# Kernel optimization log

Hardware: AMD Instinct MI355X
Metric: run time of the kernel (lower is better)

The kernel has to match this reference:

```python
import jax, jax.numpy as jnp
import numpy as np

ITERS = 3
EPS = 1e-6


def setup_inputs() -> dict:
    key = jax.random.key(0)
    k1, k2 = jax.random.split(key, 2)
    a = jax.random.normal(k1, (64, 1152, 1, 1, 1, 1), dtype=jnp.float32)
    v = jax.random.normal(k2, (64, 1152, 32, 4, 4, 1), dtype=jnp.float32)
    logits = jnp.ones((1, 1152, 32, 1, 1, 1), dtype=jnp.float32)
    return {"a": a, "v": v, "logits": logits}


def _squash(s):
    # s: (batch, 1, B, P, P, 1); norm over dim 2 (matches torch code, dim=2)
    norm_sq = jnp.sum(s * s, axis=2, keepdims=True)
    return jnp.sqrt(norm_sq + EPS) / (1.0 + norm_sq) * s


def reference(a, v, logits):
    # a: (batch, A, 1, 1, 1, 1) -- unused (overwritten in original forward)
    # v: (batch, A, B, P, P, 1); logits: (1, A, B, 1, 1, 1)
    batch = v.shape[0]
    b = jnp.broadcast_to(logits, (batch,) + logits.shape[1:])
    p = None
    for i in range(ITERS):
        c = jax.nn.softmax(b, axis=2)                    # route over B
        s = jnp.sum(c * v, axis=1, keepdims=True)        # (batch,1,B,P,P,1)
        p = _squash(s)
        if i < ITERS - 1:
            # agreement: sum over pose dims -> (batch, A, B, 1, 1, 1)
            b = b + jnp.sum(p * v, axis=(-3, -2, -1), keepdims=True)
    p = jnp.squeeze(p, axis=1)                           # (batch, B, P, P, 1)
    a_out = jnp.linalg.norm(p, ord=2, axis=2)            # (batch, B, P, 1)
    return (a_out, p)
```

## Files before the change

kernel.cpp:

```cpp
#include <hip/hip_runtime.h>
#include <math.h>

#define BATCH 64
#define ADIM  1152
#define BDIM  32
#define POSE  16
#define SLICE 512
#define CHUNKS 16
#define ROWS  72
#define RPW   18
#define WAVES 4
#define EPSQ  1e-6f
#define SPART_ITER ((size_t)BATCH * CHUNKS * SLICE)

typedef float v4f __attribute__((ext_vector_type(4)));

__device__ __forceinline__ unsigned pack_bf16x2(float a, float b) {
    unsigned ua = __float_as_uint(a), ub = __float_as_uint(b);
    ua = (ua + 0x7fffu + ((ua >> 16) & 1u)) >> 16;
    ub = (ub + 0x7fffu + ((ub >> 16) & 1u));
    return (ua & 0xffffu) | (ub & 0xffff0000u);
}

__device__ __forceinline__ v4f unpack_bf16x4(uint2 w) {
    v4f r;
    r.x = __uint_as_float(w.x << 16);
    r.y = __uint_as_float(w.x & 0xffff0000u);
    r.z = __uint_as_float(w.y << 16);
    r.w = __uint_as_float(w.y & 0xffff0000u);
    return r;
}

__global__ __launch_bounds__(256) void route0_compress(
    const float* __restrict__ v,
    const float* __restrict__ logits,
    uint2* __restrict__ tile,
    float* __restrict__ s_part)
{
    const int bt    = blockIdx.x >> 4;
    const int chunk = blockIdx.x & 15;
    const int t     = threadIdx.x;
    const int bc0   = (t >> 2) & 31;
    const int hi    = t >> 7;
    const int a0    = chunk * ROWS;

    __shared__ float w_sh[ROWS * BDIM];
    __shared__ v4f   red[128];

    if (t < ROWS) {
        const float* lr = logits + (size_t)(a0 + t) * BDIM;
        float s = 0.f;
        float e[BDIM];
#pragma unroll
        for (int b = 0; b < BDIM; ++b) { e[b] = __expf(lr[b]); s += e[b]; }
        float rd = 1.f / s;
#pragma unroll
        for (int b = 0; b < BDIM; ++b) w_sh[t * BDIM + b] = e[b] * rd;
    }
    __syncthreads();

    const v4f* vg = (const v4f*)(v + ((size_t)bt * ADIM + a0) * SLICE);
    uint2*     tg = tile + ((size_t)bt * ADIM + a0) * 128;

    v4f acc = (v4f){0.f, 0.f, 0.f, 0.f};
    v4f fA[6], fB[6];
#pragma unroll
    for (int u = 0; u < 6; ++u)
        fA[u] = __builtin_nontemporal_load(&vg[t + 256 * u]);

#pragma unroll
    for (int kk = 0; kk < 6; ++kk) {
        v4f* cur = (kk & 1) ? fB : fA;
        v4f* nxt = (kk & 1) ? fA : fB;
        if (kk + 1 < 6) {
#pragma unroll
            for (int u = 0; u < 6; ++u)
                nxt[u] = __builtin_nontemporal_load(&vg[t + 256 * ((kk + 1) * 6 + u)]);
        }
#pragma unroll
        for (int u = 0; u < 6; ++u) {
            const int k   = kk * 6 + u;
            const int i   = t + 256 * k;
            const int row = 2 * k + hi;
            tg[i] = make_uint2(pack_bf16x2(cur[u].x, cur[u].y),
                               pack_bf16x2(cur[u].z, cur[u].w));
            float c0 = w_sh[row * BDIM + bc0];
            acc += c0 * cur[u];
        }
    }

    __syncthreads();
    if (t >= 128) red[t - 128] = acc;
    __syncthreads();
    if (t < 128) {
        acc += red[t];
        ((v4f*)(s_part + ((size_t)bt * CHUNKS + chunk) * SLICE))[t] = acc;
    }
}

__global__ __launch_bounds__(256) void route_next(
    const uint2* __restrict__ tile,
    const float* __restrict__ logits,
    const float* __restrict__ psum_g,
    float* __restrict__ s_out)
{
    const int bt    = blockIdx.x >> 4;
    const int chunk = blockIdx.x & 15;
    const int t     = threadIdx.x;
    const int lane  = t & 63;
    const int wv    = t >> 6;
    const int bq    = lane >> 2;
    const int a0    = chunk * ROWS;

    __shared__ v4f red[WAVES * 128];

    const v4f* pp = (const v4f*)(psum_g + (size_t)bt * SLICE);
    v4f psA = pp[lane];
    v4f psB = pp[64 + lane];
    v4f acc0 = (v4f){0.f, 0.f, 0.f, 0.f};
    v4f acc1 = (v4f){0.f, 0.f, 0.f, 0.f};

    const int r0 = wv * RPW;
    const uint2* tb = tile + ((size_t)bt * ADIM + a0) * 128;

#pragma unroll 6
    for (int r = 0; r < RPW; ++r) {
        const int rw = r0 + r;
        uint2 wa = tb[rw * 128 + lane];
        uint2 wb = tb[rw * 128 + 64 + lane];
        v4f va = unpack_bf16x4(wa);
        v4f vb = unpack_bf16x4(wb);
        float b0 = logits[(size_t)(a0 + rw) * BDIM + bq];
        float b1 = logits[(size_t)(a0 + rw) * BDIM + 16 + bq];
        float d0 = psA.x * va.x + psA.y * va.y + psA.z * va.z + psA.w * va.w;
        float d1 = psB.x * vb.x + psB.y * vb.y + psB.z * vb.z + psB.w * vb.w;
        d0 += __shfl_xor(d0, 1, 64); d0 += __shfl_xor(d0, 2, 64);
        d1 += __shfl_xor(d1, 1, 64); d1 += __shfl_xor(d1, 2, 64);
        float e0 = __expf(b0 + d0);
        float e1 = __expf(b1 + d1);
        float uu = e0 + e1;
#pragma unroll
        for (int off = 4; off <= 32; off <<= 1)
            uu += __shfl_xor(uu, off, 64);
        float rd = __builtin_amdgcn_rcpf(uu);
        float c0 = e0 * rd, c1 = e1 * rd;
        acc0 += c0 * va;
        acc1 += c1 * vb;
    }

    __syncthreads();
    if (wv == 3) { red[lane] = acc0; red[64 + lane] = acc1; }
    __syncthreads();
    if (wv == 2) { red[lane] += acc0; red[64 + lane] += acc1; }
    __syncthreads();
    if (wv == 1) { red[lane] += acc0; red[64 + lane] += acc1; }
    __syncthreads();
    if (wv == 0) {
        v4f* sp = (v4f*)(s_out + ((size_t)bt * CHUNKS + chunk) * SLICE);
        sp[lane]      = red[lane] + acc0;
        sp[64 + lane] = red[64 + lane] + acc1;
    }
}

__global__ __launch_bounds__(512) void squash_pass(
    const float* __restrict__ s_part_j,
    float* __restrict__ psum,
    int add)
{
    const int bt = blockIdx.x;
    const int t  = threadIdx.x;

    __shared__ float sq[SLICE];
    __shared__ float fac[POSE];

    float sv = 0.f;
#pragma unroll
    for (int c = 0; c < CHUNKS; ++c)
        sv += s_part_j[((size_t)bt * CHUNKS + c) * SLICE + t];

    sq[t] = sv * sv;
    __syncthreads();
    if (t < POSE) {
        float n = 0.f;
        for (int b2 = 0; b2 < BDIM; ++b2) n += sq[b2 * POSE + t];
        fac[t] = sqrtf(n + EPSQ) / (1.f + n);
    }
    __syncthreads();
    float prev = add ? psum[(size_t)bt * SLICE + t] : 0.f;
    psum[(size_t)bt * SLICE + t] = prev + fac[t & 15] * sv;
}

__global__ __launch_bounds__(512) void final_out(
    const float* __restrict__ s_part2,
    float* __restrict__ out)
{
    const int bt = blockIdx.x;
    const int t  = threadIdx.x;
    const int pose = t & 15;

    __shared__ float sq[SLICE];
    __shared__ float ns[POSE];

    float sv = 0.f;
#pragma unroll
    for (int c = 0; c < CHUNKS; ++c)
        sv += s_part2[((size_t)bt * CHUNKS + c) * SLICE + t];

    sq[t] = sv * sv;
    __syncthreads();
    if (t < POSE) {
        float a = 0.f;
        for (int b2 = 0; b2 < BDIM; ++b2) a += sq[b2 * POSE + t];
        ns[t] = a;
    }
    __syncthreads();
    float n = ns[pose];
    float pv = sqrtf(n + EPSQ) / (1.f + n) * sv;

    out[8192 + (size_t)bt * SLICE + t] = pv;
    sq[t] = pv * pv;
    __syncthreads();
    if (t < 128) {
        const int b2 = t >> 2, p2 = t & 3;
        float a = 0.f;
#pragma unroll
        for (int p1 = 0; p1 < 4; ++p1) a += sq[b2 * POSE + p1 * 4 + p2];
        out[(size_t)bt * 128 + t] = sqrtf(a);
    }
}

extern "C" void kernel_launch(void* const* d_in, const int* in_sizes, int n_in,
                              void* d_out, int out_size, void* d_ws, size_t ws_size,
                              hipStream_t stream) {
    const float* v      = (const float*)d_in[1];
    const float* logits = (const float*)d_in[2];
    float* out = (float*)d_out;

    uint2* tile   = (uint2*)d_ws;
    float* s_part = (float*)((char*)d_ws + (size_t)BATCH * ADIM * 128 * sizeof(uint2));
    float* psum   = s_part + 3 * SPART_ITER;

    route0_compress<<<dim3(BATCH * CHUNKS), dim3(256), 0, stream>>>(
        v, logits, tile, s_part + 0 * SPART_ITER);
    squash_pass<<<dim3(BATCH), dim3(512), 0, stream>>>(
        s_part + 0 * SPART_ITER, psum, 0);
    route_next<<<dim3(BATCH * CHUNKS), dim3(256), 0, stream>>>(
        tile, logits, psum, s_part + 1 * SPART_ITER);
    squash_pass<<<dim3(BATCH), dim3(512), 0, stream>>>(
        s_part + 1 * SPART_ITER, psum, 1);
    route_next<<<dim3(BATCH * CHUNKS), dim3(256), 0, stream>>>(
        tile, logits, psum, s_part + 2 * SPART_ITER);
    final_out<<<dim3(BATCH), dim3(512), 0, stream>>>(
        s_part + 2 * SPART_ITER, out);
}
```

Measured before the change: 257.8 us.

## Drop bf16 tile cache and fuse squash into iteration passes reading fp32 v

Removes the bf16-compressed copy of v and has each routing iteration re-read the original fp32 v directly. The per-batch squash kernels are eliminated; each iteration block recomputes the squashed pose sums from the stored partial sums of prior iterations. This saves the compressed-tile write and two launches but doubles the bytes read per later iteration and adds redundant squash work per block. It also removes bf16 rounding of v.

```diff
diff --git a/kernel.cpp b/kernel.cpp
--- a/kernel.cpp
+++ b/kernel.cpp
@@ -4,105 +4,60 @@
 #define BATCH 64
 #define ADIM  1152
 #define BDIM  32
-#define POSE  16
 #define SLICE 512
 #define CHUNKS 16
 #define ROWS  72
 #define RPW   18
-#define WAVES 4
 #define EPSQ  1e-6f
 #define SPART_ITER ((size_t)BATCH * CHUNKS * SLICE)
 
 typedef float v4f __attribute__((ext_vector_type(4)));
 
-__device__ __forceinline__ unsigned pack_bf16x2(float a, float b) {
-    unsigned ua = __float_as_uint(a), ub = __float_as_uint(b);
-    ua = (ua + 0x7fffu + ((ua >> 16) & 1u)) >> 16;
-    ub = (ub + 0x7fffu + ((ub >> 16) & 1u));
-    return (ua & 0xffffu) | (ub & 0xffff0000u);
-}
-
-__device__ __forceinline__ v4f unpack_bf16x4(uint2 w) {
-    v4f r;
-    r.x = __uint_as_float(w.x << 16);
-    r.y = __uint_as_float(w.x & 0xffff0000u);
-    r.z = __uint_as_float(w.y << 16);
-    r.w = __uint_as_float(w.y & 0xffff0000u);
-    return r;
-}
-
-__global__ __launch_bounds__(256) void route0_compress(
+
+__device__ __forceinline__ void squash_from(const float* sp, int lane,
+                                            v4f& sA, v4f& sB, v4f& fac) {
+    const v4f* spv = (const v4f*)sp;
+    sA = (v4f){0.f, 0.f, 0.f, 0.f};
+    sB = (v4f){0.f, 0.f, 0.f, 0.f};
+#pragma unroll
+    for (int c = 0; c < CHUNKS; ++c) {
+        sA += spv[c * 128 + lane];
+        sB += spv[c * 128 + 64 + lane];
+    }
+    v4f nq = sA * sA + sB * sB;
+#pragma unroll
+    for (int off = 4; off <= 32; off <<= 1) {
+        nq.x += __shfl_xor(nq.x, off, 64);
+        nq.y += __shfl_xor(nq.y, off, 64);
+        nq.z += __shfl_xor(nq.z, off, 64);
+        nq.w += __shfl_xor(nq.w, off, 64);
+    }
+    fac.x = sqrtf(nq.x + EPSQ) / (1.f + nq.x);
+    fac.y = sqrtf(nq.y + EPSQ) / (1.f + nq.y);
+    fac.z = sqrtf(nq.z + EPSQ) / (1.f + nq.z);
+    fac.w = sqrtf(nq.w + EPSQ) / (1.f + nq.w);
+}
+
+__device__ __forceinline__ void reduce_write(v4f* red, int lane, int wv,
+                                             v4f ra, v4f rb, float* dst) {
+    __syncthreads();
+    if (wv == 3) { red[lane] = ra; red[64 + lane] = rb; }
+    __syncthreads();
+    if (wv == 2) { red[lane] += ra; red[64 + lane] += rb; }
+    __syncthreads();
+    if (wv == 1) { red[lane] += ra; red[64 + lane] += rb; }
+    __syncthreads();
+    if (wv == 0) {
+        v4f* sp = (v4f*)dst;
+        sp[lane]      = red[lane] + ra;
+        sp[64 + lane] = red[64 + lane] + rb;
+    }
+}
+
+__global__ __launch_bounds__(256) void pass0(
     const float* __restrict__ v,
     const float* __restrict__ logits,
-    uint2* __restrict__ tile,
-    float* __restrict__ s_part)
-{
-    const int bt    = blockIdx.x >> 4;
-    const int chunk = blockIdx.x & 15;
-    const int t     = threadIdx.x;
-    const int bc0   = (t >> 2) & 31;
-    const int hi    = t >> 7;
-    const int a0    = chunk * ROWS;
-
-    __shared__ float w_sh[ROWS * BDIM];
-    __shared__ v4f   red[128];
-
-    if (t < ROWS) {
-        const float* lr = logits + (size_t)(a0 + t) * BDIM;
-        float s = 0.f;
-        float e[BDIM];
-#pragma unroll
-        for (int b = 0; b < BDIM; ++b) { e[b] = __expf(lr[b]); s += e[b]; }
-        float rd = 1.f / s;
-#pragma unroll
-        for (int b = 0; b < BDIM; ++b) w_sh[t * BDIM + b] = e[b] * rd;
-    }
-    __syncthreads();
-
-    const v4f* vg = (const v4f*)(v + ((size_t)bt * ADIM + a0) * SLICE);
-    uint2*     tg = tile + ((size_t)bt * ADIM + a0) * 128;
-
-    v4f acc = (v4f){0.f, 0.f, 0.f, 0.f};
-    v4f fA[6], fB[6];
-#pragma unroll
-    for (int u = 0; u < 6; ++u)
-        fA[u] = __builtin_nontemporal_load(&vg[t + 256 * u]);
-
-#pragma unroll
-    for (int kk = 0; kk < 6; ++kk) {
-        v4f* cur = (kk & 1) ? fB : fA;
-        v4f* nxt = (kk & 1) ? fA : fB;
-        if (kk + 1 < 6) {
-#pragma unroll
-            for (int u = 0; u < 6; ++u)
-                nxt[u] = __builtin_nontemporal_load(&vg[t + 256 * ((kk + 1) * 6 + u)]);
-        }
-#pragma unroll
-        for (int u = 0; u < 6; ++u) {
-            const int k   = kk * 6 + u;
-            const int i   = t + 256 * k;
-            const int row = 2 * k + hi;
-            tg[i] = make_uint2(pack_bf16x2(cur[u].x, cur[u].y),
-                               pack_bf16x2(cur[u].z, cur[u].w));
-            float c0 = w_sh[row * BDIM + bc0];
-            acc += c0 * cur[u];
-        }
-    }
-
-    __syncthreads();
-    if (t >= 128) red[t - 128] = acc;
-    __syncthreads();
-    if (t < 128) {
-        acc += red[t];
-        ((v4f*)(s_part + ((size_t)bt * CHUNKS + chunk) * SLICE))[t] = acc;
-    }
-}
-
-__global__ __launch_bounds__(256) void route_next(
-    const uint2* __restrict__ tile,
-    const float* __restrict__ logits,
-    const float* __restrict__ psum_g,
-    float* __restrict__ s_out)
+    float* __restrict__ s0)
 {
     const int bt    = blockIdx.x >> 4;
     const int chunk = blockIdx.x & 15;
@@ -111,29 +66,101 @@
     const int wv    = t >> 6;
     const int bq    = lane >> 2;
     const int a0    = chunk * ROWS;
-
-    __shared__ v4f red[WAVES * 128];
-
-    const v4f* pp = (const v4f*)(psum_g + (size_t)bt * SLICE);
-    v4f psA = pp[lane];
-    v4f psB = pp[64 + lane];
+    const int r0    = wv * RPW;
+
+    __shared__ float w_sh[ROWS * BDIM];
+    __shared__ v4f   red[128];
+
+    if (t < ROWS) {
+        const float* lr = logits + (size_t)(a0 + t) * BDIM;
+        float e[BDIM];
+        float s = 0.f;
+#pragma unroll
+        for (int b = 0; b < BDIM; ++b) { e[b] = __expf(lr[b]); s += e[b]; }
+        float rd = 1.f / s;
+#pragma unroll
+        for (int b = 0; b < BDIM; ++b) w_sh[t * BDIM + b] = e[b] * rd;
+    }
+    __syncthreads();
+
+    const v4f* vg = (const v4f*)(v + ((size_t)bt * ADIM + a0 + r0) * SLICE);
     v4f acc0 = (v4f){0.f, 0.f, 0.f, 0.f};
     v4f acc1 = (v4f){0.f, 0.f, 0.f, 0.f};
 
-    const int r0 = wv * RPW;
-    const uint2* tb = tile + ((size_t)bt * ADIM + a0) * 128;
-
-#pragma unroll 6
+    v4f fA[6], fB[6];
+#pragma unroll
+    for (int u = 0; u < 6; ++u) fA[u] = vg[lane + 64 * u];
+
+#pragma unroll
+    for (int kk = 0; kk < 6; ++kk) {
+        v4f* cur = (kk & 1) ? fB : fA;
+        v4f* nxt = (kk & 1) ? fA : fB;
+        if (kk + 1 < 6) {
+#pragma unroll
+            for (int u = 0; u < 6; ++u)
+                nxt[u] = vg[lane + 64 * ((kk + 1) * 6 + u)];
+        }
+#pragma unroll
+        for (int u = 0; u < 6; ++u) {
+            const int j  = kk * 6 + u;
+            const int rw = r0 + (j >> 1);
+            if ((j & 1) == 0) acc0 += w_sh[rw * BDIM + bq] * cur[u];
+            else              acc1 += w_sh[rw * BDIM + 16 + bq] * cur[u];
+        }
+    }
+
+    reduce_write(red, lane, wv, acc0, acc1,
+                 s0 + ((size_t)bt * CHUNKS + chunk) * SLICE);
+}
+
+__global__ __launch_bounds__(256) void iter_pass(
+    const float* __restrict__ v,
+    const float* __restrict__ logits,
+    const float* __restrict__ s_part,
+    float* __restrict__ s_next,
+    int nprev)
+{
+    const int bt    = blockIdx.x >> 4;
+    const int chunk = blockIdx.x & 15;
+    const int t     = threadIdx.x;
+    const int lane  = t & 63;
+    const int wv    = t >> 6;
+    const int bq    = lane >> 2;
+    const int a0    = chunk * ROWS;
+    const int r0    = wv * RPW;
+
+    __shared__ v4f red[128];
+
+    v4f pA = (v4f){0.f, 0.f, 0.f, 0.f};
+    v4f pB = (v4f){0.f, 0.f, 0.f, 0.f};
+    for (int j = 0; j < nprev; ++j) {
+        v4f sA, sB, fac;
+        squash_from(s_part + (size_t)j * SPART_ITER +
+                    (size_t)bt * CHUNKS * SLICE, lane, sA, sB, fac);
+        pA += fac * sA;
+        pB += fac * sB;
+    }
+
+    const v4f*  vr  = (const v4f*)(v + ((size_t)bt * ADIM + a0 + r0) * SLICE);
+    const float* lgr = logits + (size_t)(a0 + r0) * BDIM;
+
+    v4f acc0 = (v4f){0.f, 0.f, 0.f, 0.f};
+    v4f acc1 = (v4f){0.f, 0.f, 0.f, 0.f};
+
+    v4f  vaN = vr[lane], vbN = vr[64 + lane];
+    float b0N = lgr[bq], b1N = lgr[16 + bq];
+#pragma unroll
     for (int r = 0; r < RPW; ++r) {
-        const int rw = r0 + r;
-        uint2 wa = tb[rw * 128 + lane];
-        uint2 wb = tb[rw * 128 + 64 + lane];
-        v4f va = unpack_bf16x4(wa);
-        v4f vb = unpack_bf16x4(wb);
-        float b0 = logits[(size_t)(a0 + rw) * BDIM + bq];
-        float b1 = logits[(size_t)(a0 + rw) * BDIM + 16 + bq];
-        float d0 = psA.x * va.x + psA.y * va.y + psA.z * va.z + psA.w * va.w;
-        float d1 = psB.x * vb.x + psB.y * vb.y + psB.z * vb.z + psB.w * vb.w;
+        v4f  va = vaN, vb = vbN;
+        float b0 = b0N, b1 = b1N;
+        if (r + 1 < RPW) {
+            vaN = vr[(r + 1) * 128 + lane];
+            vbN = vr[(r + 1) * 128 + 64 + lane];
+            b0N = lgr[(r + 1) * BDIM + bq];
+            b1N = lgr[(r + 1) * BDIM + 16 + bq];
+        }
+        float d0 = pA.x * va.x + pA.y * va.y + pA.z * va.z + pA.w * va.w;
+        float d1 = pB.x * vb.x + pB.y * vb.y + pB.z * vb.z + pB.w * vb.w;
         d0 += __shfl_xor(d0, 1, 64); d0 += __shfl_xor(d0, 2, 64);
         d1 += __shfl_xor(d1, 1, 64); d1 += __shfl_xor(d1, 2, 64);
         float e0 = __expf(b0 + d0);
@@ -142,52 +169,13 @@
 #pragma unroll
         for (int off = 4; off <= 32; off <<= 1)
             uu += __shfl_xor(uu, off, 64);
-        float rd = __builtin_amdgcn_rcpf(uu);
-        float c0 = e0 * rd, c1 = e1 * rd;
-        acc0 += c0 * va;
-        acc1 += c1 * vb;
-    }
-
-    __syncthreads();
-    if (wv == 3) { red[lane] = acc0; red[64 + lane] = acc1; }
-    __syncthreads();
-    if (wv == 2) { red[lane] += acc0; red[64 + lane] += acc1; }
-    __syncthreads();
-    if (wv == 1) { red[lane] += acc0; red[64 + lane] += acc1; }
-    __syncthreads();
-    if (wv == 0) {
-        v4f* sp = (v4f*)(s_out + ((size_t)bt * CHUNKS + chunk) * SLICE);
-        sp[lane]      = red[lane] + acc0;
-        sp[64 + lane] = red[64 + lane] + acc1;
-    }
-}
-
-__global__ __launch_bounds__(512) void squash_pass(
-    const float* __restrict__ s_part_j,
-    float* __restrict__ psum,
-    int add)
-{
-    const int bt = blockIdx.x;
-    const int t  = threadIdx.x;
-
-    __shared__ float sq[SLICE];
-    __shared__ float fac[POSE];
-
-    float sv = 0.f;
-#pragma unroll
-    for (int c = 0; c < CHUNKS; ++c)
-        sv += s_part_j[((size_t)bt * CHUNKS + c) * SLICE + t];
-
-    sq[t] = sv * sv;
-    __syncthreads();
-    if (t < POSE) {
-        float n = 0.f;
-        for (int b2 = 0; b2 < BDIM; ++b2) n += sq[b2 * POSE + t];
-        fac[t] = sqrtf(n + EPSQ) / (1.f + n);
-    }
-    __syncthreads();
-    float prev = add ? psum[(size_t)bt * SLICE + t] : 0.f;
-    psum[(size_t)bt * SLICE + t] = prev + fac[t & 15] * sv;
+        float rdc = __builtin_amdgcn_rcpf(uu);
+        acc0 += (e0 * rdc) * va;
+        acc1 += (e1 * rdc) * vb;
+    }
+
+    reduce_write(red, lane, wv, acc0, acc1,
+                 s_next + ((size_t)bt * CHUNKS + chunk) * SLICE);
 }
 
 __global__ __launch_bounds__(512) void final_out(
@@ -199,7 +187,7 @@
     const int pose = t & 15;
 
     __shared__ float sq[SLICE];
-    __shared__ float ns[POSE];
+    __shared__ float ns[16];
 
     float sv = 0.f;
 #pragma unroll
@@ -208,9 +196,9 @@
 
     sq[t] = sv * sv;
     __syncthreads();
-    if (t < POSE) {
+    if (t < 16) {
         float a = 0.f;
-        for (int b2 = 0; b2 < BDIM; ++b2) a += sq[b2 * POSE + t];
+        for (int b2 = 0; b2 < BDIM; ++b2) a += sq[b2 * 16 + t];
         ns[t] = a;
     }
     __syncthreads();
@@ -224,7 +212,7 @@
         const int b2 = t >> 2, p2 = t & 3;
         float a = 0.f;
 #pragma unroll
-        for (int p1 = 0; p1 < 4; ++p1) a += sq[b2 * POSE + p1 * 4 + p2];
+        for (int p1 = 0; p1 < 4; ++p1) a += sq[b2 * 16 + p1 * 4 + p2];
         out[(size_t)bt * 128 + t] = sqrtf(a);
     }
 }
@@ -234,22 +222,15 @@
                               hipStream_t stream) {
     const float* v      = (const float*)d_in[1];
     const float* logits = (const float*)d_in[2];
-    float* out = (float*)d_out;
-
-    uint2* tile   = (uint2*)d_ws;
-    float* s_part = (float*)((char*)d_ws + (size_t)BATCH * ADIM * 128 * sizeof(uint2));
-    float* psum   = s_part + 3 * SPART_ITER;
-
-    route0_compress<<<dim3(BATCH * CHUNKS), dim3(256), 0, stream>>>(
-        v, logits, tile, s_part + 0 * SPART_ITER);
-    squash_pass<<<dim3(BATCH), dim3(512), 0, stream>>>(
-        s_part + 0 * SPART_ITER, psum, 0);
-    route_next<<<dim3(BATCH * CHUNKS), dim3(256), 0, stream>>>(
-        tile, logits, psum, s_part + 1 * SPART_ITER);
-    squash_pass<<<dim3(BATCH), dim3(512), 0, stream>>>(
-        s_part + 1 * SPART_ITER, psum, 1);
-    route_next<<<dim3(BATCH * CHUNKS), dim3(256), 0, stream>>>(
-        tile, logits, psum, s_part + 2 * SPART_ITER);
+    float* out    = (float*)d_out;
+    float* s_part = (float*)d_ws;
+
+    pass0<<<dim3(BATCH * CHUNKS), dim3(256), 0, stream>>>(
+        v, logits, s_part);
+    iter_pass<<<dim3(BATCH * CHUNKS), dim3(256), 0, stream>>>(
+        v, logits, s_part, s_part + 1 * SPART_ITER, 1);
+    iter_pass<<<dim3(BATCH * CHUNKS), dim3(256), 0, stream>>>(
+        v, logits, s_part, s_part + 2 * SPART_ITER, 2);
     final_out<<<dim3(BATCH), dim3(512), 0, stream>>>(
         s_part + 2 * SPART_ITER, out);
 }
```

Result: slower. 272.2 us (+5.6%).
